# Optimization experiments

Measured on AMD Instinct MI355X. Metric: run time of the kernel, lower is better.

Reference implementation:

```python
import jax, jax.numpy as jnp
import numpy as np

GAMMA = 0.99
EPS = 1e-07


def setup_inputs() -> dict:
    key = jax.random.key(0)
    k1, k2, k3 = jax.random.split(key, 3)
    V, D = 8192, 256
    b, s = 8, 16
    x = jax.random.normal(k1, (b, D, s, s, s), dtype=jnp.float32)
    weight = jax.random.normal(k2, (V, D), dtype=jnp.float32)
    N = jnp.zeros((V,), dtype=jnp.float32)
    z_avg = jax.random.normal(k3, (V, D), dtype=jnp.float32)
    return {"x": x, "weight": weight, "N": N, "z_avg": z_avg}


def reference(x, weight, N, z_avg):
    V, D = weight.shape
    b, c, x1, x2, x3 = x.shape
    # (b, c, x1, x2, x3) -> (b*x1*x2*x3, D), channels last
    flat = jnp.transpose(x, (0, 2, 3, 4, 1)).reshape(-1, D)
    # pairwise squared L2 distances: ||z||^2 - 2 z.W^T + ||W||^2
    dists = (
        jnp.sum(flat * flat, axis=1, keepdims=True)
        - 2.0 * (flat @ weight.T)
        + jnp.sum(weight * weight, axis=1)[None, :]
    )
    idx = jnp.argmin(dists, axis=1)  # same tie-break (first) as torch.max(-d)
    quant = weight[idx].reshape(b, x1, x2, x3, D)
    quant = jnp.transpose(quant, (0, 4, 1, 2, 3))  # back to (b, c, x1, x2, x3)

    # EMA cluster statistics (training-mode update) via scatter-reduce,
    # equivalent to the torch one-hot matmuls encode_onehot.sum(0) and
    # flat_inputs.T @ encode_onehot.
    counts = jax.ops.segment_sum(jnp.ones(flat.shape[0], dtype=flat.dtype), idx, num_segments=V)
    enc_sum = jax.ops.segment_sum(flat, idx, num_segments=V)  # (V, D)
    new_N = GAMMA * N + (1.0 - GAMMA) * counts
    new_z_avg = GAMMA * z_avg + (1.0 - GAMMA) * enc_sum
    n = jnp.sum(new_N)
    w = (new_N + EPS) / (n + V * EPS) * n
    new_weight = new_z_avg / w[:, None]

    quant_st = jax.lax.stop_gradient(quant - x) + x  # straight-through
    quant_diff = jnp.mean(jnp.square(x - jax.lax.stop_gradient(quant)))
    enc_idx = idx.reshape(b, x1, x2, x3)
    return quant_st, enc_idx, quant_diff, new_N, new_z_avg, new_weight
```

## Files before the change

### kernel.cpp

```cpp
#include <hip/hip_runtime.h>

#define V_CODES 8192
#define D_DIM   256
#define SPATIAL 4096
#define M_ROWS  32768
#define NELEM   8388608

static constexpr float GAMMA_F = 0.99f;
static constexpr float OMG_F   = (float)(1.0 - 0.99);
static constexpr float EPS_F   = 1e-7f;
static constexpr float VEPS_F  = (float)(8192 * 1e-7);

static constexpr size_t OFF_QUANT = 0;
static constexpr size_t OFF_IDX   = 8388608;
static constexpr size_t OFF_QDIFF = 8421376;
static constexpr size_t OFF_NN    = 8421377;
static constexpr size_t OFF_ZAVG  = 8429569;
static constexpr size_t OFF_W     = 10526721;

typedef _Float16 f16x8 __attribute__((ext_vector_type(8)));
typedef float    f32x4 __attribute__((ext_vector_type(4)));

#define GLL(gp, lp) __builtin_amdgcn_global_load_lds( \
    (const __attribute__((address_space(1))) unsigned int*)(gp), \
    (__attribute__((address_space(3))) unsigned int*)(lp), 16, 0, 0)

__global__ void k_wnorm(const float* __restrict__ W, float* __restrict__ wnorm) {
    int v = blockIdx.x * 4 + (threadIdx.x >> 6);
    int lane = threadIdx.x & 63;
    float4 w4 = *(const float4*)(W + (size_t)v * D_DIM + lane * 4);
    float s = w4.x * w4.x + w4.y * w4.y + w4.z * w4.z + w4.w * w4.w;
    #pragma unroll
    for (int m = 32; m > 0; m >>= 1) s += __shfl_xor(s, m, 64);
    if (lane == 0) wnorm[v] = s;
}

__global__ void k_split_w(const float* __restrict__ W, _Float16* __restrict__ Wh,
                          _Float16* __restrict__ Wl) {
    size_t i8 = ((size_t)blockIdx.x * 256 + threadIdx.x) * 8;
    float4 a = *(const float4*)(W + i8);
    float4 b = *(const float4*)(W + i8 + 4);
    float v[8] = {a.x, a.y, a.z, a.w, b.x, b.y, b.z, b.w};
    f16x8 hi, lo;
    #pragma unroll
    for (int j = 0; j < 8; j++) {
        _Float16 h = (_Float16)v[j];
        hi[j] = h;
        lo[j] = (_Float16)(v[j] - (float)h);
    }
    *(f16x8*)(Wh + i8) = hi;
    *(f16x8*)(Wl + i8) = lo;
}

__global__ void k_split_x(const float* __restrict__ X, _Float16* __restrict__ Xh,
                          _Float16* __restrict__ Xl) {
    int bid  = blockIdx.x;
    int lane = threadIdx.x & 63;
    int kg   = (bid & 1) * 4 + (threadIdx.x >> 6);
    int m    = (bid >> 1) * 64 + lane;
    int b  = m >> 12;
    int sp = m & 4095;
    const float* src = X + (size_t)b * (D_DIM * SPATIAL) + (size_t)(kg * 32) * SPATIAL + sp;
    float v[32];
    #pragma unroll
    for (int j = 0; j < 32; j++) v[j] = src[(size_t)j * SPATIAL];
    _Float16* dh = Xh + (size_t)m * D_DIM + kg * 32;
    _Float16* dl = Xl + (size_t)m * D_DIM + kg * 32;
    #pragma unroll
    for (int c = 0; c < 4; c++) {
        f16x8 hi, lo;
        #pragma unroll
        for (int j = 0; j < 8; j++) {
            float x = v[c * 8 + j];
            _Float16 h = (_Float16)x;
            hi[j] = h;
            lo[j] = (_Float16)(x - (float)h);
        }
        *(f16x8*)(dh + c * 8) = hi;
        *(f16x8*)(dl + c * 8) = lo;
    }
}

__device__ inline unsigned long long packkey(float s, int v) {
    unsigned u = __float_as_uint(s);
    u = (u & 0x80000000u) ? ~u : (u | 0x80000000u);
    return ((unsigned long long)u << 32) | (unsigned)v;
}

__global__ __launch_bounds__(256, 2) void k_mfma_argmin(
        const _Float16* __restrict__ Xh, const _Float16* __restrict__ Xl,
        const _Float16* __restrict__ Wh, const _Float16* __restrict__ Wl,
        const float* __restrict__ wnorm, unsigned long long* __restrict__ best) {
    __shared__ __align__(16) _Float16 lds[16384];
    const int tid  = threadIdx.x;
    const int wid  = tid >> 6;
    const int lane = tid & 63;
    const int wy = wid >> 1, wx = wid & 1;
    const int lrow = lane & 15, lq = lane >> 4;
    const int m0 = blockIdx.y * 128;
    const int v0 = blockIdx.x * 128;

    f32x4 acc[4][4] = {};

    const _Float16* planes[4] = {Xh, Xl, Wh, Wl};
    const _Float16* P = planes[wid];
    const int rowb = (wid < 2 ? m0 : v0) + lrow;

    for (int k0 = 0; k0 < D_DIM; k0 += 32) {
        __syncthreads();
        #pragma unroll
        for (int sub = 0; sub < 8; sub++) {
            const _Float16* g = P + (size_t)(rowb + sub * 16) * D_DIM + k0 + lq * 8;
            GLL(g, &lds[(wid * 8 + sub) * 512]);
        }
        __syncthreads();
        f16x8 ah[4], al[4], bh[4], bl[4];
        #pragma unroll
        for (int i = 0; i < 4; i++) {
            ah[i] = *(const f16x8*)&lds[(      wy * 4 + i) * 512 + lane * 8];
            al[i] = *(const f16x8*)&lds[( 8 + wy * 4 + i) * 512 + lane * 8];
            bh[i] = *(const f16x8*)&lds[(16 + wx * 4 + i) * 512 + lane * 8];
            bl[i] = *(const f16x8*)&lds[(24 + wx * 4 + i) * 512 + lane * 8];
        }
        #pragma unroll
        for (int mi = 0; mi < 4; mi++)
            #pragma unroll
            for (int vi = 0; vi < 4; vi++) {
                acc[mi][vi] = __builtin_amdgcn_mfma_f32_16x16x32_f16(ah[mi], bh[vi], acc[mi][vi], 0, 0, 0);
                acc[mi][vi] = __builtin_amdgcn_mfma_f32_16x16x32_f16(al[mi], bh[vi], acc[mi][vi], 0, 0, 0);
                acc[mi][vi] = __builtin_amdgcn_mfma_f32_16x16x32_f16(ah[mi], bl[vi], acc[mi][vi], 0, 0, 0);
            }
    }

    float wnv[4];
    #pragma unroll
    for (int vi = 0; vi < 4; vi++) wnv[vi] = wnorm[v0 + (wx * 4 + vi) * 16 + lrow];

    #pragma unroll
    for (int mi = 0; mi < 4; mi++) {
        #pragma unroll
        for (int r = 0; r < 4; r++) {
            unsigned long long k = ~0ull;
            #pragma unroll
            for (int vi = 0; vi < 4; vi++) {
                int v = v0 + (wx * 4 + vi) * 16 + lrow;
                float s = wnv[vi] - 2.0f * acc[mi][vi][r];
                unsigned long long key = packkey(s, v);
                k = key < k ? key : k;
            }
            #pragma unroll
            for (int msk = 1; msk < 16; msk <<= 1) {
                unsigned long long o = __shfl_xor(k, msk, 64);
                k = o < k ? o : k;
            }
            if (lrow == 0) {
                int m = m0 + (wy * 4 + mi) * 16 + lq * 4 + r;
                atomicMin(&best[m], k);
            }
        }
    }
}

__global__ void k_count(const unsigned long long* __restrict__ best,
                        int* __restrict__ counts, float* __restrict__ out) {
    int m = blockIdx.x * 256 + threadIdx.x;
    int v = (int)(unsigned)(best[m] & 0xFFFFFFFFull);
    atomicAdd(&counts[v], 1);
    out[OFF_IDX + m] = (float)v;
}

__global__ void k_prefix(const int* __restrict__ counts, int* __restrict__ offsets,
                         int* __restrict__ cursor) {
    __shared__ int tsum[256];
    int t = threadIdx.x;
    int local[32];
    int s = 0;
    #pragma unroll
    for (int i = 0; i < 32; i++) { local[i] = s; s += counts[t * 32 + i]; }
    tsum[t] = s;
    __syncthreads();
    if (t == 0) {
        int run = 0;
        for (int i = 0; i < 256; i++) { int c = tsum[i]; tsum[i] = run; run += c; }
    }
    __syncthreads();
    int base = tsum[t];
    #pragma unroll
    for (int i = 0; i < 32; i++) {
        int o = base + local[i];
        offsets[t * 32 + i] = o;
        cursor[t * 32 + i]  = o;
    }
}

__global__ void k_fill(const unsigned long long* __restrict__ best,
                       int* __restrict__ cursor, int* __restrict__ bin) {
    int m = blockIdx.x * 256 + threadIdx.x;
    int v = (int)(unsigned)(best[m] & 0xFFFFFFFFull);
    int pos = atomicAdd(&cursor[v], 1);
    bin[pos] = m;
}

__global__ void k_codes(const _Float16* __restrict__ Xh, const _Float16* __restrict__ Xl,
                        const float* __restrict__ N, const float* __restrict__ zavg,
                        const int* __restrict__ counts, const int* __restrict__ offsets,
                        const int* __restrict__ bin, float* __restrict__ out) {
    int v = blockIdx.x;
    int d = threadIdx.x;
    int cnt = counts[v];
    int off = offsets[v];
    float s = 0.0f;
    for (int r = 0; r < cnt; r++) {
        int m = bin[off + r];
        s += (float)Xh[(size_t)m * D_DIM + d] + (float)Xl[(size_t)m * D_DIM + d];
    }
    out[OFF_ZAVG + (size_t)v * D_DIM + d] = GAMMA_F * zavg[(size_t)v * D_DIM + d] + OMG_F * s;
    if (d == 0) out[OFF_NN + v] = GAMMA_F * N[v] + OMG_F * (float)cnt;
}

__global__ void k_quant(const float* __restrict__ X, const float* __restrict__ W,
                        const unsigned long long* __restrict__ best, float* __restrict__ out,
                        float* __restrict__ ws_scal) {
    int e4 = blockIdx.x * 256 + threadIdx.x;
    int e  = e4 * 4;
    int sp = e & 4095;
    int bd = e >> 12;
    int d  = bd & 255;
    int b  = bd >> 8;
    int mb = b * SPATIAL + sp;
    float4 x4 = *(const float4*)(X + e);
    float q[4];
    float p = 0.0f;
    #pragma unroll
    for (int j = 0; j < 4; j++) {
        int v = (int)(unsigned)(best[mb + j] & 0xFFFFFFFFull);
        float wv = W[(size_t)v * D_DIM + d];
        float xv = (j == 0) ? x4.x : (j == 1) ? x4.y : (j == 2) ? x4.z : x4.w;
        q[j] = (wv - xv) + xv;
        float df = xv - wv;
        p = fmaf(df, df, p);
    }
    *(float4*)(out + OFF_QUANT + e) = make_float4(q[0], q[1], q[2], q[3]);
    #pragma unroll
    for (int msk = 32; msk > 0; msk >>= 1) p += __shfl_xor(p, msk, 64);
    __shared__ float red[4];
    int lane = threadIdx.x & 63, w = threadIdx.x >> 6;
    if (lane == 0) red[w] = p;
    __syncthreads();
    if (threadIdx.x == 0)
        atomicAdd(ws_scal, red[0] + red[1] + red[2] + red[3]);
}

__global__ void k_finalize_n(const float* __restrict__ outNN, float* __restrict__ ws_scal,
                             float* __restrict__ out_qdiff) {
    __shared__ float red[256];
    float s = 0.0f;
    for (int v = threadIdx.x; v < V_CODES; v += 256) s += outNN[v];
    red[threadIdx.x] = s;
    __syncthreads();
    #pragma unroll
    for (int t = 128; t > 0; t >>= 1) {
        if (threadIdx.x < t) red[threadIdx.x] += red[threadIdx.x + t];
        __syncthreads();
    }
    if (threadIdx.x == 0) {
        ws_scal[1] = red[0];
        out_qdiff[0] = ws_scal[0] * (1.0f / 8388608.0f);
    }
}

__global__ void k_weight(const float* __restrict__ zavg_out, const float* __restrict__ nn_out,
                         const float* __restrict__ ws_scal, float* __restrict__ out_w) {
    int i = blockIdx.x * 256 + threadIdx.x;
    int v = i >> 8;
    float n = ws_scal[1];
    float w = (nn_out[v] + EPS_F) / (n + VEPS_F) * n;
    out_w[i] = zavg_out[i] / w;
}

extern "C" void kernel_launch(void* const* d_in, const int* in_sizes, int n_in,
                              void* d_out, int out_size, void* d_ws, size_t ws_size,
                              hipStream_t stream) {
    const float* x    = (const float*)d_in[0];
    const float* w    = (const float*)d_in[1];
    const float* N    = (const float*)d_in[2];
    const float* zavg = (const float*)d_in[3];
    float* out = (float*)d_out;
    char*  wsb = (char*)d_ws;

    float* ws_scal   = (float*)wsb;
    int*   ws_counts = (int*)(wsb + 64);
    float* ws_wnorm  = (float*)(wsb + 32832);
    int*   ws_off    = (int*)(wsb + 65600);
    int*   ws_cur    = (int*)(wsb + 98368);
    int*   ws_bin    = (int*)(wsb + 131136);
    unsigned long long* ws_best = (unsigned long long*)(wsb + 262208);
    _Float16* Xh = (_Float16*)(wsb + 524352);
    _Float16* Xl = (_Float16*)(wsb + 524352 + 16777216);
    _Float16* Wh = (_Float16*)(wsb + 524352 + 2 * 16777216);
    _Float16* Wl = (_Float16*)(wsb + 524352 + 2 * 16777216 + 4194304);

    hipMemsetAsync(wsb, 0, 32832, stream);
    hipMemsetAsync(ws_best, 0xFF, (size_t)M_ROWS * 8, stream);

    k_wnorm  <<<V_CODES / 4, 256, 0, stream>>>(w, ws_wnorm);
    k_split_w<<<(V_CODES * D_DIM) / (256 * 8), 256, 0, stream>>>(w, Wh, Wl);
    k_split_x<<<1024, 256, 0, stream>>>(x, Xh, Xl);

    dim3 grid(V_CODES / 128, M_ROWS / 128);
    k_mfma_argmin<<<grid, 256, 0, stream>>>(Xh, Xl, Wh, Wl, ws_wnorm, ws_best);

    k_count  <<<M_ROWS / 256, 256, 0, stream>>>(ws_best, ws_counts, out);
    k_prefix <<<1, 256, 0, stream>>>(ws_counts, ws_off, ws_cur);
    k_fill   <<<M_ROWS / 256, 256, 0, stream>>>(ws_best, ws_cur, ws_bin);
    k_codes  <<<V_CODES, 256, 0, stream>>>(Xh, Xl, N, zavg, ws_counts, ws_off, ws_bin, out);
    k_quant  <<<NELEM / (256 * 4), 256, 0, stream>>>(x, w, ws_best, out, ws_scal);

    k_finalize_n<<<1, 256, 0, stream>>>(out + OFF_NN, ws_scal, out + OFF_QDIFF);
    k_weight <<<(V_CODES * D_DIM) / 256, 256, 0, stream>>>(out + OFF_ZAVG, out + OFF_NN, ws_scal, out + OFF_W);
}
```

Measured before the change: 960.4 us.

## Enlarge argmin GEMM tile to 256x256 with double-buffered LDS prefetch

Rewrites the split-fp16 MFMA distance/argmin kernel to use 512-thread blocks on 256x256 tiles, so each loaded operand is reused across more output. The global-to-LDS loads for the next k-slice are double-buffered and issued in between MFMA phases, with s_setprio raising priority during the math, so copy latency overlaps compute. The cost is 128KB of LDS and 8x4 accumulators per wave, which raises register pressure, could cap occupancy below the requested 2 blocks per CU, and reduces the number of blocks in the grid.

```diff
diff --git a/kernel.cpp b/kernel.cpp
--- a/kernel.cpp
+++ b/kernel.cpp
@@ -87,63 +87,85 @@
     return ((unsigned long long)u << 32) | (unsigned)v;
 }
 
-__global__ __launch_bounds__(256, 2) void k_mfma_argmin(
+__global__ __launch_bounds__(512, 2) void k_mfma_argmin(
         const _Float16* __restrict__ Xh, const _Float16* __restrict__ Xl,
         const _Float16* __restrict__ Wh, const _Float16* __restrict__ Wl,
         const float* __restrict__ wnorm, unsigned long long* __restrict__ best) {
-    __shared__ __align__(16) _Float16 lds[16384];
+    __shared__ __align__(16) _Float16 lds[65536];
     const int tid  = threadIdx.x;
     const int wid  = tid >> 6;
     const int lane = tid & 63;
-    const int wy = wid >> 1, wx = wid & 1;
     const int lrow = lane & 15, lq = lane >> 4;
-    const int m0 = blockIdx.y * 128;
-    const int v0 = blockIdx.x * 128;
-
-    f32x4 acc[4][4] = {};
-
-    const _Float16* planes[4] = {Xh, Xl, Wh, Wl};
-    const _Float16* P = planes[wid];
-    const int rowb = (wid < 2 ? m0 : v0) + lrow;
-
-    for (int k0 = 0; k0 < D_DIM; k0 += 32) {
-        __syncthreads();
+    const int wy = wid >> 2, wx = wid & 3;
+    const int m0 = blockIdx.y * 256;
+    const int v0 = blockIdx.x * 256;
+
+    const _Float16* const planesArr[4] = {Xh, Xl, Wh, Wl};
+    const _Float16* const SP = planesArr[wid >> 1];
+    const int sgbase = (wid & 1) * 8;
+    const int srow = (wid < 4 ? m0 : v0) + sgbase * 16 + lrow;
+    const int lgrp = ((wid >> 1) << 4) + sgbase;
+
+    f32x4 acc[8][4] = {};
+
+#define STAGE(bf, kt, s) GLL(SP + (size_t)(srow + (s) * 16) * D_DIM + (kt) * 32 + lq * 8, \
+                             &lds[((size_t)(((bf) << 6) + lgrp + (s))) << 9])
+#define LDF(bf, grp, sg) (*(const f16x8*)&lds[(((size_t)((((bf) << 6) + ((grp) << 4) + (sg)))) << 9) + (lane << 3)])
+
+    #pragma unroll
+    for (int s = 0; s < 8; ++s) STAGE(0, 0, s);
+    __syncthreads();
+
+    #pragma unroll 1
+    for (int t = 0; t < 8; ++t) {
+        const int cur = t & 1, nxt = cur ^ 1;
+        f16x8 bh[4], bl[4];
         #pragma unroll
-        for (int sub = 0; sub < 8; sub++) {
-            const _Float16* g = P + (size_t)(rowb + sub * 16) * D_DIM + k0 + lq * 8;
-            GLL(g, &lds[(wid * 8 + sub) * 512]);
+        for (int p = 0; p < 4; ++p) {
+            f16x8 a0h = LDF(cur, 0, wy * 8 + 2 * p);
+            f16x8 a1h = LDF(cur, 0, wy * 8 + 2 * p + 1);
+            f16x8 a0l = LDF(cur, 1, wy * 8 + 2 * p);
+            f16x8 a1l = LDF(cur, 1, wy * 8 + 2 * p + 1);
+            if (p == 0) {
+                #pragma unroll
+                for (int vi = 0; vi < 4; ++vi) {
+                    bh[vi] = LDF(cur, 2, wx * 4 + vi);
+                    bl[vi] = LDF(cur, 3, wx * 4 + vi);
+                }
+            }
+            if (p < 2 && t < 7) {
+                #pragma unroll
+                for (int s = 0; s < 4; ++s) STAGE(nxt, t + 1, p * 4 + s);
+            }
+            __builtin_amdgcn_s_barrier();
+            __builtin_amdgcn_s_setprio(1);
+            #pragma unroll
+            for (int vi = 0; vi < 4; ++vi) {
+                acc[2*p][vi]   = __builtin_amdgcn_mfma_f32_16x16x32_f16(a0h, bh[vi], acc[2*p][vi], 0, 0, 0);
+                acc[2*p][vi]   = __builtin_amdgcn_mfma_f32_16x16x32_f16(a0l, bh[vi], acc[2*p][vi], 0, 0, 0);
+                acc[2*p][vi]   = __builtin_amdgcn_mfma_f32_16x16x32_f16(a0h, bl[vi], acc[2*p][vi], 0, 0, 0);
+                acc[2*p+1][vi] = __builtin_amdgcn_mfma_f32_16x16x32_f16(a1h, bh[vi], acc[2*p+1][vi], 0, 0, 0);
+                acc[2*p+1][vi] = __builtin_amdgcn_mfma_f32_16x16x32_f16(a1l, bh[vi], acc[2*p+1][vi], 0, 0, 0);
+                acc[2*p+1][vi] = __builtin_amdgcn_mfma_f32_16x16x32_f16(a1h, bl[vi], acc[2*p+1][vi], 0, 0, 0);
+            }
+            __builtin_amdgcn_s_setprio(0);
+            __builtin_amdgcn_s_barrier();
         }
         __syncthreads();
-        f16x8 ah[4], al[4], bh[4], bl[4];
+    }
+
+    float wnv[4];
+    #pragma unroll
+    for (int vi = 0; vi < 4; ++vi) wnv[vi] = wnorm[v0 + wx * 64 + vi * 16 + lrow];
+
+    #pragma unroll
+    for (int mi = 0; mi < 8; ++mi) {
         #pragma unroll
-        for (int i = 0; i < 4; i++) {
-            ah[i] = *(const f16x8*)&lds[(      wy * 4 + i) * 512 + lane * 8];
-            al[i] = *(const f16x8*)&lds[( 8 + wy * 4 + i) * 512 + lane * 8];
-            bh[i] = *(const f16x8*)&lds[(16 + wx * 4 + i) * 512 + lane * 8];
-            bl[i] = *(const f16x8*)&lds[(24 + wx * 4 + i) * 512 + lane * 8];
-        }
-        #pragma unroll
-        for (int mi = 0; mi < 4; mi++)
-            #pragma unroll
-            for (int vi = 0; vi < 4; vi++) {
-                acc[mi][vi] = __builtin_amdgcn_mfma_f32_16x16x32_f16(ah[mi], bh[vi], acc[mi][vi], 0, 0, 0);
-                acc[mi][vi] = __builtin_amdgcn_mfma_f32_16x16x32_f16(al[mi], bh[vi], acc[mi][vi], 0, 0, 0);
-                acc[mi][vi] = __builtin_amdgcn_mfma_f32_16x16x32_f16(ah[mi], bl[vi], acc[mi][vi], 0, 0, 0);
-            }
-    }
-
-    float wnv[4];
-    #pragma unroll
-    for (int vi = 0; vi < 4; vi++) wnv[vi] = wnorm[v0 + (wx * 4 + vi) * 16 + lrow];
-
-    #pragma unroll
-    for (int mi = 0; mi < 4; mi++) {
-        #pragma unroll
-        for (int r = 0; r < 4; r++) {
+        for (int r = 0; r < 4; ++r) {
             unsigned long long k = ~0ull;
             #pragma unroll
-            for (int vi = 0; vi < 4; vi++) {
-                int v = v0 + (wx * 4 + vi) * 16 + lrow;
+            for (int vi = 0; vi < 4; ++vi) {
+                int v = v0 + wx * 64 + vi * 16 + lrow;
                 float s = wnv[vi] - 2.0f * acc[mi][vi][r];
                 unsigned long long key = packkey(s, v);
                 k = key < k ? key : k;
@@ -153,12 +175,12 @@
                 unsigned long long o = __shfl_xor(k, msk, 64);
                 k = o < k ? o : k;
             }
-            if (lrow == 0) {
-                int m = m0 + (wy * 4 + mi) * 16 + lq * 4 + r;
-                atomicMin(&best[m], k);
-            }
+            if (lrow == 0)
+                atomicMin(&best[m0 + wy * 128 + mi * 16 + lq * 4 + r], k);
         }
     }
+#undef STAGE
+#undef LDF
 }
 
 __global__ void k_count(const unsigned long long* __restrict__ best,
@@ -307,8 +329,8 @@
     k_split_w<<<(V_CODES * D_DIM) / (256 * 8), 256, 0, stream>>>(w, Wh, Wl);
     k_split_x<<<1024, 256, 0, stream>>>(x, Xh, Xl);
 
-    dim3 grid(V_CODES / 128, M_ROWS / 128);
-    k_mfma_argmin<<<grid, 256, 0, stream>>>(Xh, Xl, Wh, Wl, ws_wnorm, ws_best);
+    dim3 grid(V_CODES / 256, M_ROWS / 256);
+    k_mfma_argmin<<<grid, 512, 0, stream>>>(Xh, Xl, Wh, Wl, ws_wnorm, ws_best);
 
     k_count  <<<M_ROWS / 256, 256, 0, stream>>>(ws_best, ws_counts, out);
     k_prefix <<<1, 256, 0, stream>>>(ws_counts, ws_off, ws_cur);
```

New measurement: 969.8 us. About the same (+1.0%).

## Switch argmin GEMM to 32x32x16 MFMA tiles with reorganized LDS layout

Applied to the files above, without the earlier changes.

Rewrites the distance-GEMM inner loop to use 32x32x16 f16 MFMA instructions instead of 16x16x32, with a new LDS staging layout and a 2x2 accumulator grid per wave. It also raises the launch-bounds occupancy target to 3 blocks per CU and adds s_setprio around the MFMA bursts. The argmin epilogue is adapted to the 32x32 output layout, with a wider shuffle reduction. The aim is fewer MFMA issues and LDS reads per flop, at the cost of register pressure from the higher occupancy target and a costlier epilogue reduction.

```diff
diff --git a/kernel.cpp b/kernel.cpp
--- a/kernel.cpp
+++ b/kernel.cpp
@@ -18,8 +18,9 @@
 static constexpr size_t OFF_ZAVG  = 8429569;
 static constexpr size_t OFF_W     = 10526721;
 
-typedef _Float16 f16x8 __attribute__((ext_vector_type(8)));
-typedef float    f32x4 __attribute__((ext_vector_type(4)));
+typedef _Float16 f16x8  __attribute__((ext_vector_type(8)));
+typedef float    f32x4  __attribute__((ext_vector_type(4)));
+typedef float    f32x16 __attribute__((ext_vector_type(16)));
 
 #define GLL(gp, lp) __builtin_amdgcn_global_load_lds( \
     (const __attribute__((address_space(1))) unsigned int*)(gp), \
@@ -87,7 +88,7 @@
     return ((unsigned long long)u << 32) | (unsigned)v;
 }
 
-__global__ __launch_bounds__(256, 2) void k_mfma_argmin(
+__global__ __launch_bounds__(256, 3) void k_mfma_argmin(
         const _Float16* __restrict__ Xh, const _Float16* __restrict__ Xl,
         const _Float16* __restrict__ Wh, const _Float16* __restrict__ Wl,
         const float* __restrict__ wnorm, unsigned long long* __restrict__ best) {
@@ -95,70 +96,85 @@
     const int tid  = threadIdx.x;
     const int wid  = tid >> 6;
     const int lane = tid & 63;
+    const int l31  = lane & 31, lq2 = lane >> 5;
     const int wy = wid >> 1, wx = wid & 1;
-    const int lrow = lane & 15, lq = lane >> 4;
     const int m0 = blockIdx.y * 128;
     const int v0 = blockIdx.x * 128;
 
-    f32x4 acc[4][4] = {};
-
-    const _Float16* planes[4] = {Xh, Xl, Wh, Wl};
-    const _Float16* P = planes[wid];
-    const int rowb = (wid < 2 ? m0 : v0) + lrow;
-
+    const _Float16* const PL[4] = {Xh, Xl, Wh, Wl};
+
+    f32x16 acc[2][2] = {};
+
+#define LDF(O, p, rg, kg) (*(const f16x8*)&lds[((size_t)(((O) << 4) + ((p) << 3) + ((rg) << 1) + (kg)) << 9) + (lane << 3)])
+
+    #pragma unroll 1
     for (int k0 = 0; k0 < D_DIM; k0 += 32) {
         __syncthreads();
         #pragma unroll
-        for (int sub = 0; sub < 8; sub++) {
-            const _Float16* g = P + (size_t)(rowb + sub * 16) * D_DIM + k0 + lq * 8;
-            GLL(g, &lds[(wid * 8 + sub) * 512]);
+        for (int j = 0; j < 8; ++j) {
+            const int ss = wid * 8 + j;
+            const int O  = ss >> 4, p = (ss >> 3) & 1, rg = (ss >> 1) & 3, kg = ss & 1;
+            const _Float16* g = PL[O * 2 + p]
+                + (size_t)((O ? v0 : m0) + rg * 32 + l31) * D_DIM
+                + k0 + kg * 16 + lq2 * 8;
+            GLL(g, &lds[(size_t)ss << 9]);
         }
         __syncthreads();
-        f16x8 ah[4], al[4], bh[4], bl[4];
         #pragma unroll
-        for (int i = 0; i < 4; i++) {
-            ah[i] = *(const f16x8*)&lds[(      wy * 4 + i) * 512 + lane * 8];
-            al[i] = *(const f16x8*)&lds[( 8 + wy * 4 + i) * 512 + lane * 8];
-            bh[i] = *(const f16x8*)&lds[(16 + wx * 4 + i) * 512 + lane * 8];
-            bl[i] = *(const f16x8*)&lds[(24 + wx * 4 + i) * 512 + lane * 8];
+        for (int kg = 0; kg < 2; ++kg) {
+            f16x8 ah0 = LDF(0, 0, wy * 2 + 0, kg);
+            f16x8 ah1 = LDF(0, 0, wy * 2 + 1, kg);
+            f16x8 al0 = LDF(0, 1, wy * 2 + 0, kg);
+            f16x8 al1 = LDF(0, 1, wy * 2 + 1, kg);
+            f16x8 bh0 = LDF(1, 0, wx * 2 + 0, kg);
+            f16x8 bh1 = LDF(1, 0, wx * 2 + 1, kg);
+            f16x8 bl0 = LDF(1, 1, wx * 2 + 0, kg);
+            f16x8 bl1 = LDF(1, 1, wx * 2 + 1, kg);
+            __builtin_amdgcn_s_setprio(1);
+            acc[0][0] = __builtin_amdgcn_mfma_f32_32x32x16_f16(ah0, bh0, acc[0][0], 0, 0, 0);
+            acc[0][1] = __builtin_amdgcn_mfma_f32_32x32x16_f16(ah0, bh1, acc[0][1], 0, 0, 0);
+            acc[1][0] = __builtin_amdgcn_mfma_f32_32x32x16_f16(ah1, bh0, acc[1][0], 0, 0, 0);
+            acc[1][1] = __builtin_amdgcn_mfma_f32_32x32x16_f16(ah1, bh1, acc[1][1], 0, 0, 0);
+            acc[0][0] = __builtin_amdgcn_mfma_f32_32x32x16_f16(al0, bh0, acc[0][0], 0, 0, 0);
+            acc[0][1] = __builtin_amdgcn_mfma_f32_32x32x16_f16(al0, bh1, acc[0][1], 0, 0, 0);
+            acc[1][0] = __builtin_amdgcn_mfma_f32_32x32x16_f16(al1, bh0, acc[1][0], 0, 0, 0);
+            acc[1][1] = __builtin_amdgcn_mfma_f32_32x32x16_f16(al1, bh1, acc[1][1], 0, 0, 0);
+            acc[0][0] = __builtin_amdgcn_mfma_f32_32x32x16_f16(ah0, bl0, acc[0][0], 0, 0, 0);
+            acc[0][1] = __builtin_amdgcn_mfma_f32_32x32x16_f16(ah0, bl1, acc[0][1], 0, 0, 0);
+            acc[1][0] = __builtin_amdgcn_mfma_f32_32x32x16_f16(ah1, bl0, acc[1][0], 0, 0, 0);
+            acc[1][1] = __builtin_amdgcn_mfma_f32_32x32x16_f16(ah1, bl1, acc[1][1], 0, 0, 0);
+            __builtin_amdgcn_s_setprio(0);
         }
+    }
+
+    float wnv[2];
+    #pragma unroll
+    for (int vi = 0; vi < 2; ++vi) wnv[vi] = wnorm[v0 + wx * 64 + vi * 32 + l31];
+
+    #pragma unroll
+    for (int mi = 0; mi < 2; ++mi) {
         #pragma unroll
-        for (int mi = 0; mi < 4; mi++)
-            #pragma unroll
-            for (int vi = 0; vi < 4; vi++) {
-                acc[mi][vi] = __builtin_amdgcn_mfma_f32_16x16x32_f16(ah[mi], bh[vi], acc[mi][vi], 0, 0, 0);
-                acc[mi][vi] = __builtin_amdgcn_mfma_f32_16x16x32_f16(al[mi], bh[vi], acc[mi][vi], 0, 0, 0);
-                acc[mi][vi] = __builtin_amdgcn_mfma_f32_16x16x32_f16(ah[mi], bl[vi], acc[mi][vi], 0, 0, 0);
-            }
-    }
-
-    float wnv[4];
-    #pragma unroll
-    for (int vi = 0; vi < 4; vi++) wnv[vi] = wnorm[v0 + (wx * 4 + vi) * 16 + lrow];
-
-    #pragma unroll
-    for (int mi = 0; mi < 4; mi++) {
-        #pragma unroll
-        for (int r = 0; r < 4; r++) {
+        for (int r = 0; r < 16; ++r) {
             unsigned long long k = ~0ull;
             #pragma unroll
-            for (int vi = 0; vi < 4; vi++) {
-                int v = v0 + (wx * 4 + vi) * 16 + lrow;
+            for (int vi = 0; vi < 2; ++vi) {
+                int v = v0 + wx * 64 + vi * 32 + l31;
                 float s = wnv[vi] - 2.0f * acc[mi][vi][r];
                 unsigned long long key = packkey(s, v);
                 k = key < k ? key : k;
             }
             #pragma unroll
-            for (int msk = 1; msk < 16; msk <<= 1) {
+            for (int msk = 1; msk < 32; msk <<= 1) {
                 unsigned long long o = __shfl_xor(k, msk, 64);
                 k = o < k ? o : k;
             }
-            if (lrow == 0) {
-                int m = m0 + (wy * 4 + mi) * 16 + lq * 4 + r;
+            if (l31 == 0) {
+                int m = m0 + wy * 64 + mi * 32 + (r & 3) + 8 * (r >> 2) + 4 * lq2;
                 atomicMin(&best[m], k);
             }
         }
     }
+#undef LDF
 }
 
 __global__ void k_count(const unsigned long long* __restrict__ best,
```

New measurement: 1.030 ms. 1.07x slower.

## Load MFMA operands directly from global memory instead of staging through LDS

Applied to the files above, without the earlier changes.

The argmin GEMM kernel no longer stages X and W fp16 hi/lo tiles into shared memory with global_load_lds and barriers. Each wave now loads its own fragments straight from global memory, with the K loop fully unrolled, and raises wave priority around the MFMA block. This removes the LDS round trip and the per-step block syncs. In exchange, wave pairs that share rows fetch the same data redundantly through L2/L1, and global load latency is no longer hidden by a shared staging buffer.

```diff
diff --git a/kernel.cpp b/kernel.cpp
--- a/kernel.cpp
+++ b/kernel.cpp
@@ -18,12 +18,8 @@
 static constexpr size_t OFF_ZAVG  = 8429569;
 static constexpr size_t OFF_W     = 10526721;
 
-typedef _Float16 f16x8 __attribute__((ext_vector_type(8)));
-typedef float    f32x4 __attribute__((ext_vector_type(4)));
-
-#define GLL(gp, lp) __builtin_amdgcn_global_load_lds( \
-    (const __attribute__((address_space(1))) unsigned int*)(gp), \
-    (__attribute__((address_space(3))) unsigned int*)(lp), 16, 0, 0)
+typedef _Float16 f16x8  __attribute__((ext_vector_type(8)));
+typedef float    f32x4  __attribute__((ext_vector_type(4)));
 
 __global__ void k_wnorm(const float* __restrict__ W, float* __restrict__ wnorm) {
     int v = blockIdx.x * 4 + (threadIdx.x >> 6);
@@ -91,58 +87,60 @@
         const _Float16* __restrict__ Xh, const _Float16* __restrict__ Xl,
         const _Float16* __restrict__ Wh, const _Float16* __restrict__ Wl,
         const float* __restrict__ wnorm, unsigned long long* __restrict__ best) {
-    __shared__ __align__(16) _Float16 lds[16384];
     const int tid  = threadIdx.x;
     const int wid  = tid >> 6;
     const int lane = tid & 63;
+    const int lrow = lane & 15, lq = lane >> 4;
     const int wy = wid >> 1, wx = wid & 1;
-    const int lrow = lane & 15, lq = lane >> 4;
     const int m0 = blockIdx.y * 128;
     const int v0 = blockIdx.x * 128;
 
+    const _Float16 *pah[4], *pal[4], *pbh[4], *pbl[4];
+    #pragma unroll
+    for (int i = 0; i < 4; ++i) {
+        const size_t ar = (size_t)(m0 + (wy * 4 + i) * 16 + lrow) * D_DIM + lq * 8;
+        const size_t br = (size_t)(v0 + (wx * 4 + i) * 16 + lrow) * D_DIM + lq * 8;
+        pah[i] = Xh + ar;
+        pal[i] = Xl + ar;
+        pbh[i] = Wh + br;
+        pbl[i] = Wl + br;
+    }
+
     f32x4 acc[4][4] = {};
 
-    const _Float16* planes[4] = {Xh, Xl, Wh, Wl};
-    const _Float16* P = planes[wid];
-    const int rowb = (wid < 2 ? m0 : v0) + lrow;
-
-    for (int k0 = 0; k0 < D_DIM; k0 += 32) {
-        __syncthreads();
-        #pragma unroll
-        for (int sub = 0; sub < 8; sub++) {
-            const _Float16* g = P + (size_t)(rowb + sub * 16) * D_DIM + k0 + lq * 8;
-            GLL(g, &lds[(wid * 8 + sub) * 512]);
-        }
-        __syncthreads();
+    #pragma unroll
+    for (int t = 0; t < 8; ++t) {
         f16x8 ah[4], al[4], bh[4], bl[4];
         #pragma unroll
-        for (int i = 0; i < 4; i++) {
-            ah[i] = *(const f16x8*)&lds[(      wy * 4 + i) * 512 + lane * 8];
-            al[i] = *(const f16x8*)&lds[( 8 + wy * 4 + i) * 512 + lane * 8];
-            bh[i] = *(const f16x8*)&lds[(16 + wx * 4 + i) * 512 + lane * 8];
-            bl[i] = *(const f16x8*)&lds[(24 + wx * 4 + i) * 512 + lane * 8];
+        for (int i = 0; i < 4; ++i) {
+            ah[i] = *(const f16x8*)(pah[i] + t * 32);
+            al[i] = *(const f16x8*)(pal[i] + t * 32);
+            bh[i] = *(const f16x8*)(pbh[i] + t * 32);
+            bl[i] = *(const f16x8*)(pbl[i] + t * 32);
         }
+        __builtin_amdgcn_s_setprio(1);
         #pragma unroll
-        for (int mi = 0; mi < 4; mi++)
+        for (int mi = 0; mi < 4; ++mi)
             #pragma unroll
-            for (int vi = 0; vi < 4; vi++) {
+            for (int vi = 0; vi < 4; ++vi) {
                 acc[mi][vi] = __builtin_amdgcn_mfma_f32_16x16x32_f16(ah[mi], bh[vi], acc[mi][vi], 0, 0, 0);
                 acc[mi][vi] = __builtin_amdgcn_mfma_f32_16x16x32_f16(al[mi], bh[vi], acc[mi][vi], 0, 0, 0);
                 acc[mi][vi] = __builtin_amdgcn_mfma_f32_16x16x32_f16(ah[mi], bl[vi], acc[mi][vi], 0, 0, 0);
             }
+        __builtin_amdgcn_s_setprio(0);
     }
 
     float wnv[4];
     #pragma unroll
-    for (int vi = 0; vi < 4; vi++) wnv[vi] = wnorm[v0 + (wx * 4 + vi) * 16 + lrow];
-
-    #pragma unroll
-    for (int mi = 0; mi < 4; mi++) {
+    for (int vi = 0; vi < 4; ++vi) wnv[vi] = wnorm[v0 + (wx * 4 + vi) * 16 + lrow];
+
+    #pragma unroll
+    for (int mi = 0; mi < 4; ++mi) {
         #pragma unroll
-        for (int r = 0; r < 4; r++) {
+        for (int r = 0; r < 4; ++r) {
             unsigned long long k = ~0ull;
             #pragma unroll
-            for (int vi = 0; vi < 4; vi++) {
+            for (int vi = 0; vi < 4; ++vi) {
                 int v = v0 + (wx * 4 + vi) * 16 + lrow;
                 float s = wnv[vi] - 2.0f * acc[mi][vi][r];
                 unsigned long long key = packkey(s, v);
```

Measured after the change: 1.358 ms. 1.41x slower.
